# Performance work log

Measured on AMD Instinct MI355X. Metric: run time of the kernel, lower is better.

## Reference

```python
import jax, jax.numpy as jnp
import numpy as np

B, N, C = 2, 2048, 1024
H = 16
D = C // H  # head_dim = 64
SCALE = D ** -0.5


def setup_inputs() -> dict:
    key = jax.random.key(0)
    ks = jax.random.split(key, 9)
    s = C ** -0.5  # ~ torch Linear default init scale
    return {
        "x": jax.random.normal(ks[0], (B, N, C), dtype=jnp.float32),
        "Wq": jax.random.uniform(ks[1], (C, C), jnp.float32, -s, s),
        "bq": jax.random.uniform(ks[2], (C,), jnp.float32, -s, s),
        "Wk": jax.random.uniform(ks[3], (C, C), jnp.float32, -s, s),
        "bk": jax.random.uniform(ks[4], (C,), jnp.float32, -s, s),
        "Wv": jax.random.uniform(ks[5], (C, C), jnp.float32, -s, s),
        "bv": jax.random.uniform(ks[6], (C,), jnp.float32, -s, s),
        "Wo": jax.random.uniform(ks[7], (C, C), jnp.float32, -s, s),
        "bo": jax.random.uniform(ks[8], (C,), jnp.float32, -s, s),
    }


def reference(x, Wq, bq, Wk, bk, Wv, bv, Wo, bo):
    # Projections: [B,N,C] -> [B,H,N,D]
    def split_heads(t):
        return t.reshape(B, N, H, D).transpose(0, 2, 1, 3)

    q = split_heads(x @ Wq.T + bq)
    k = split_heads(x @ Wk.T + bk)
    v = split_heads(x @ Wv.T + bv)

    scores = jnp.einsum("bhnd,bhmd->bhnm", q, k) * SCALE  # [B,H,N,N]
    attn = jax.nn.softmax(scores, axis=-1)
    out = jnp.einsum("bhnm,bhmd->bhnd", attn, v)  # [B,H,N,D]
    out = out.transpose(0, 2, 1, 3).reshape(B, N, C)
    return out @ Wo.T + bo
```

## Files before the change

### kernel.cpp

```cpp
#include <hip/hip_runtime.h>
#include <stdint.h>


typedef _Float16 h8 __attribute__((ext_vector_type(8)));
typedef _Float16 h4 __attribute__((ext_vector_type(4)));
typedef float f4 __attribute__((ext_vector_type(4)));
typedef float f16f __attribute__((ext_vector_type(16)));
typedef uint32_t u32;
typedef u32 u32x4 __attribute__((ext_vector_type(4)));

#define AS1(p) ((const __attribute__((address_space(1))) void*)(p))
#define AS3(p) ((__attribute__((address_space(3))) void*)(p))

template <int ITERS>
__device__ __forceinline__ void stage128B(const _Float16* g, int ldk, _Float16* s, int tid) {
#pragma unroll
  for (int j = 0; j < ITERS; ++j) {
    int off = j * 4096 + tid * 16;
    int row = off >> 7;
    int ch = (off >> 4) & 7;
    int gch = ch ^ (row & 7);
    __builtin_amdgcn_global_load_lds(AS1(g + row * ldk + gch * 8), AS3(s + (off >> 1)), 16, 0, 0);
  }
}

__device__ __forceinline__ void stage_v(const _Float16* g, _Float16* s, int tid) {
#pragma unroll
  for (int j = 0; j < 2; ++j) {
    int off = j * 4096 + tid * 16;
    int row = off >> 7;
    int ch = (off >> 4) & 7;
    int gch = ch ^ (row & 7);
    __builtin_amdgcn_global_load_lds(AS1(g + row * 2048 + gch * 8), AS3(s + (off >> 1)), 16, 0, 0);
  }
}
__device__ __forceinline__ void stage_k(const _Float16* g, _Float16* s, int tid) {
#pragma unroll
  for (int j = 0; j < 2; ++j) {
    int off = j * 4096 + tid * 16;
    int row = off >> 7;
    int ch = (off >> 4) & 7;
    int gch = ch ^ ((row & 3) | ((row >> 1) & 4));
    __builtin_amdgcn_global_load_lds(AS1(g + row * 64 + gch * 8), AS3(s + (off >> 1)), 16, 0, 0);
  }
}

__device__ __forceinline__ h8 frag64(const _Float16* s, int row, int g) {
  return *(const h8*)(s + row * 64 + ((g ^ (row & 7)) << 3));
}

__global__ void cvt_all(const float* __restrict__ x, const float* __restrict__ Wq,
                        const float* __restrict__ Wk, const float* __restrict__ Wv,
                        const float* __restrict__ Wo, _Float16* __restrict__ xh,
                        _Float16* __restrict__ q, _Float16* __restrict__ k,
                        _Float16* __restrict__ v, _Float16* __restrict__ o) {
  int blk = blockIdx.x;
  const float* src; _Float16* dst; int off;
  if (blk < 2048)      { src = x;  dst = xh; off = blk; }
  else if (blk < 2560) { src = Wq; dst = q;  off = blk - 2048; }
  else if (blk < 3072) { src = Wk; dst = k;  off = blk - 2560; }
  else if (blk < 3584) { src = Wv; dst = v;  off = blk - 3072; }
  else                 { src = Wo; dst = o;  off = blk - 3584; }
  int i = off * 2048 + threadIdx.x * 8;
  f4 a = *(const f4*)(src + i);
  f4 b = *(const f4*)(src + i + 4);
  h8 ov;
  ov[0] = (_Float16)a[0]; ov[1] = (_Float16)a[1]; ov[2] = (_Float16)a[2]; ov[3] = (_Float16)a[3];
  ov[4] = (_Float16)b[0]; ov[5] = (_Float16)b[1]; ov[6] = (_Float16)b[2]; ov[7] = (_Float16)b[3];
  *(h8*)(dst + i) = ov;
}

__global__ __launch_bounds__(256, 4) void gemm_qkv(
    const _Float16* __restrict__ X,
    const _Float16* __restrict__ W0, const _Float16* __restrict__ W1, const _Float16* __restrict__ W2,
    const float* __restrict__ b0, const float* __restrict__ b1, const float* __restrict__ b2,
    _Float16* __restrict__ O0, _Float16* __restrict__ O1, _Float16* __restrict__ O2) {
  __shared__ _Float16 As[128 * 64];
  __shared__ _Float16 Bs[64 * 64];

  int flat = blockIdx.x + 16 * (blockIdx.y + 32 * blockIdx.z);
  int nid = (flat & 7) * 192 + (flat >> 3);
  int z = nid >> 9;
  int rem = nid & 511;
  int by = rem >> 4, bx = rem & 15;

  const _Float16* W = (z == 0) ? W0 : (z == 1) ? W1 : W2;
  const float* bias = (z == 0) ? b0 : (z == 1) ? b1 : b2;

  int tid = threadIdx.x;
  int lane = tid & 63, wave = tid >> 6;
  int quad = lane >> 4, l15 = lane & 15;
  int wm = (wave >> 1) << 6, wn = (wave & 1) << 5;
  int m0 = by << 7, n0 = bx << 6;

  f4 acc[4][2] = {};
  for (int k0 = 0; k0 < 1024; k0 += 64) {
    stage128B<4>(X + m0 * 1024 + k0, 1024, As, tid);
    stage128B<2>(W + n0 * 1024 + k0, 1024, Bs, tid);
    __syncthreads();
#pragma unroll
    for (int ks = 0; ks < 2; ++ks) {
      h8 af[4], bf[2];
#pragma unroll
      for (int i = 0; i < 4; ++i) af[i] = frag64(As, wm + i * 16 + l15, ks * 4 + quad);
#pragma unroll
      for (int i = 0; i < 2; ++i) bf[i] = frag64(Bs, wn + i * 16 + l15, ks * 4 + quad);
#pragma unroll
      for (int mi = 0; mi < 4; ++mi)
#pragma unroll
        for (int ni = 0; ni < 2; ++ni)
          acc[mi][ni] = __builtin_amdgcn_mfma_f32_16x16x32_f16(af[mi], bf[ni], acc[mi][ni], 0, 0, 0);
    }
    __syncthreads();
  }

  if (z == 2) {
#pragma unroll
    for (int mi = 0; mi < 4; ++mi) {
#pragma unroll
      for (int ni = 0; ni < 2; ++ni) {
        int o = n0 + wn + ni * 16 + l15;
        float bv = bias[o];
        int h = o >> 6, dd = o & 63;
        int m = m0 + wm + mi * 16 + quad * 4;
        int b = m >> 11, n = m & 2047;
        h4 v;
#pragma unroll
        for (int r = 0; r < 4; ++r) v[r] = (_Float16)(acc[mi][ni][r] + bv);
        *(h4*)(O2 + (((b * 16 + h) * 64 + dd) * 2048 + n)) = v;
      }
    }
  } else {
    float scale = (z == 0) ? 0.125f * 1.44269504089f : 1.0f;
    _Float16* Out = (z == 0) ? O0 : O1;
#pragma unroll
    for (int mi = 0; mi < 4; ++mi) {
#pragma unroll
      for (int ni = 0; ni < 2; ++ni) {
        int o = n0 + wn + ni * 16 + l15;
        float bv = bias[o];
        int h = o >> 6, d = o & 63;
#pragma unroll
        for (int r = 0; r < 4; ++r) {
          int m = m0 + wm + mi * 16 + quad * 4 + r;
          int b = m >> 11, n = m & 2047;
          float v = (acc[mi][ni][r] + bv) * scale;
          Out[(((b * 16 + h) * 2048 + n) << 6) + d] = (_Float16)v;
        }
      }
    }
  }
}

__global__ __launch_bounds__(256, 3) void gemm_out(
    const _Float16* __restrict__ A, const _Float16* __restrict__ W,
    const float* __restrict__ bias, float* __restrict__ Out) {
  __shared__ _Float16 As[128 * 64];
  __shared__ _Float16 Bs[64 * 64];
  int tid = threadIdx.x;
  int lane = tid & 63, wave = tid >> 6;
  int quad = lane >> 4, l15 = lane & 15;
  int wm = (wave >> 1) << 6, wn = (wave & 1) << 5;

  int flat = blockIdx.x + (blockIdx.y << 4);
  int nid = (flat & 7) * 64 + (flat >> 3);
  int n0 = (nid & 15) << 6;
  int m0 = (nid >> 4) << 7;

  f4 acc[4][2] = {};
  for (int k0 = 0; k0 < 1024; k0 += 64) {
    stage128B<4>(A + m0 * 1024 + k0, 1024, As, tid);
    stage128B<2>(W + n0 * 1024 + k0, 1024, Bs, tid);
    __syncthreads();
#pragma unroll
    for (int ks = 0; ks < 2; ++ks) {
      h8 af[4], bf[2];
#pragma unroll
      for (int i = 0; i < 4; ++i) af[i] = frag64(As, wm + i * 16 + l15, ks * 4 + quad);
#pragma unroll
      for (int i = 0; i < 2; ++i) bf[i] = frag64(Bs, wn + i * 16 + l15, ks * 4 + quad);
#pragma unroll
      for (int mi = 0; mi < 4; ++mi)
#pragma unroll
        for (int ni = 0; ni < 2; ++ni)
          acc[mi][ni] = __builtin_amdgcn_mfma_f32_16x16x32_f16(af[mi], bf[ni], acc[mi][ni], 0, 0, 0);
    }
    __syncthreads();
  }
#pragma unroll
  for (int mi = 0; mi < 4; ++mi) {
#pragma unroll
    for (int ni = 0; ni < 2; ++ni) {
      int o = n0 + wn + ni * 16 + l15;
      float bv = bias[o];
#pragma unroll
      for (int r = 0; r < 4; ++r) {
        int m = m0 + wm + mi * 16 + quad * 4 + r;
        Out[m * 1024 + o] = acc[mi][ni][r] + bv;
      }
    }
  }
}

__global__ __launch_bounds__(256, 2) void attn(
    const _Float16* __restrict__ Q, const _Float16* __restrict__ Kv,
    const _Float16* __restrict__ Vt, _Float16* __restrict__ AO) {
  __shared__ _Float16 smem[6 * 4096];
  _Float16* Ksb = smem;
  _Float16* Vsb = smem + 3 * 4096;

  int tid = threadIdx.x, lane = tid & 63, wave = tid >> 6;
  int h = lane >> 5, l31 = lane & 31;
  int p = wave & 1, qg = wave >> 1;

  int flat = blockIdx.y * 16 + blockIdx.x;
  int nid = (flat & 7) * 64 + (flat >> 3);
  int bh = nid >> 4, q0 = (nid & 15) << 7;

  const _Float16* Qb = Q + (bh * 2048 + q0 + qg * 64 + l31) * 64;
  h8 qf[2][4];
#pragma unroll
  for (int qs = 0; qs < 2; ++qs)
#pragma unroll
    for (int ks4 = 0; ks4 < 4; ++ks4)
      qf[qs][ks4] = *(const h8*)(Qb + qs * 32 * 64 + ks4 * 16 + h * 8);

  int krow = (l31 & 19) | ((l31 & 4) << 1) | ((l31 & 8) >> 1);
  int kbase = (p * 32 + krow) * 64;
  int kx = (krow & 3) | ((krow >> 1) & 4);
  int vx = l31 & 7;

  const _Float16* Kb = Kv + bh * 131072;
  const _Float16* Vb = Vt + bh * 131072;
  f16f oacc[2][2] = {};
  float lsum[2] = {0.f, 0.f};

  stage_k(Kb, Ksb, tid);
  stage_v(Vb, Vsb, tid);
  stage_k(Kb + 4096, Ksb + 4096, tid);
  stage_v(Vb + 64, Vsb + 4096, tid);

  int bp = 0;
  for (int ph = 0; ph < 32; ++ph) {
    if (ph < 31) {
      asm volatile("s_waitcnt vmcnt(4)\n\ts_barrier" ::: "memory");
    } else {
      asm volatile("s_waitcnt vmcnt(0)\n\ts_barrier" ::: "memory");
    }
    const _Float16* Kst = Ksb + bp * 4096;
    const _Float16* Vst = Vsb + bp * 4096;

    f16f sacc[2] = {};
#pragma unroll
    for (int ks4 = 0; ks4 < 4; ++ks4) {
      h8 kf = *(const h8*)(Kst + kbase + (((ks4 * 2 + h) ^ kx) << 3));
      sacc[0] = __builtin_amdgcn_mfma_f32_32x32x16_f16(kf, qf[0][ks4], sacc[0], 0, 0, 0);
      sacc[1] = __builtin_amdgcn_mfma_f32_32x32x16_f16(kf, qf[1][ks4], sacc[1], 0, 0, 0);
    }

    u32 pkw[2][8];
#pragma unroll
    for (int qs = 0; qs < 2; ++qs) {
#pragma unroll
      for (int i = 0; i < 8; ++i) {
        float pa = __builtin_amdgcn_exp2f(sacc[qs][2 * i]);
        float pb = __builtin_amdgcn_exp2f(sacc[qs][2 * i + 1]);
        lsum[qs] += pa + pb;
        pkw[qs][i] = __builtin_bit_cast(u32, __builtin_amdgcn_cvt_pkrtz(pa, pb));
      }
    }

#pragma unroll
    for (int s = 0; s < 2; ++s) {
      u32x4 pw0 = {pkw[0][4 * s], pkw[0][4 * s + 1], pkw[0][4 * s + 2], pkw[0][4 * s + 3]};
      u32x4 pw1 = {pkw[1][4 * s], pkw[1][4 * s + 1], pkw[1][4 * s + 2], pkw[1][4 * s + 3]};
      h8 pb0 = __builtin_bit_cast(h8, pw0);
      h8 pb1 = __builtin_bit_cast(h8, pw1);
      int ch = (((p << 2) | (s << 1) | h) ^ vx) << 3;
#pragma unroll
      for (int dt = 0; dt < 2; ++dt) {
        h8 vf = *(const h8*)(Vst + (dt * 32 + l31) * 64 + ch);
        oacc[0][dt] = __builtin_amdgcn_mfma_f32_32x32x16_f16(vf, pb0, oacc[0][dt], 0, 0, 0);
        oacc[1][dt] = __builtin_amdgcn_mfma_f32_32x32x16_f16(vf, pb1, oacc[1][dt], 0, 0, 0);
      }
    }

    if (ph < 30) {
      int sl = bp ? bp - 1 : 2;
      stage_k(Kb + (ph + 2) * 4096, Ksb + sl * 4096, tid);
      stage_v(Vb + (ph + 2) * 64, Vsb + sl * 4096, tid);
    }
    bp = (bp == 2) ? 0 : bp + 1;
  }

  __syncthreads();
  float* cb = (float*)smem;
  if (p) {
    float* w = cb + (qg * 64 + lane) * 66;
#pragma unroll
    for (int qs = 0; qs < 2; ++qs)
#pragma unroll
      for (int dt = 0; dt < 2; ++dt)
#pragma unroll
        for (int i = 0; i < 16; ++i) w[(qs * 2 + dt) * 16 + i] = oacc[qs][dt][i];
    w[64] = lsum[0];
    w[65] = lsum[1];
  }
  __syncthreads();
  if (!p) {
    const float* r = cb + (qg * 64 + lane) * 66;
#pragma unroll
    for (int qs = 0; qs < 2; ++qs)
#pragma unroll
      for (int dt = 0; dt < 2; ++dt)
#pragma unroll
        for (int i = 0; i < 16; ++i) oacc[qs][dt][i] += r[(qs * 2 + dt) * 16 + i];
    lsum[0] += r[64];
    lsum[1] += r[65];

    int b = bh >> 4, hh = bh & 15;
#pragma unroll
    for (int qs = 0; qs < 2; ++qs) {
      float l = lsum[qs] + __shfl_xor(lsum[qs], 32);
      float inv = 1.0f / l;
      int n = q0 + qg * 64 + qs * 32 + l31;
      _Float16* base = AO + (b * 2048 + n) * 1024 + hh * 64;
#pragma unroll
      for (int dt = 0; dt < 2; ++dt) {
#pragma unroll
        for (int b2 = 0; b2 < 4; ++b2) {
          h4 o;
#pragma unroll
          for (int a = 0; a < 4; ++a) o[a] = (_Float16)(oacc[qs][dt][b2 * 4 + a] * inv);
          *(h4*)(base + dt * 32 + b2 * 8 + h * 4) = o;
        }
      }
    }
  }
}

extern "C" void kernel_launch(void* const* d_in, const int* in_sizes, int n_in,
                              void* d_out, int out_size, void* d_ws, size_t ws_size,
                              hipStream_t stream) {
  const float* x = (const float*)d_in[0];
  const float* Wq = (const float*)d_in[1];
  const float* bq = (const float*)d_in[2];
  const float* Wk = (const float*)d_in[3];
  const float* bk = (const float*)d_in[4];
  const float* Wv = (const float*)d_in[5];
  const float* bv = (const float*)d_in[6];
  const float* Wo = (const float*)d_in[7];
  const float* bo = (const float*)d_in[8];
  float* out = (float*)d_out;

  char* w = (char*)d_ws;
  _Float16* xh  = (_Float16*)(w);
  _Float16* Wqh = (_Float16*)(w + (8u << 20));
  _Float16* Wkh = (_Float16*)(w + (10u << 20));
  _Float16* Wvh = (_Float16*)(w + (12u << 20));
  _Float16* Woh = (_Float16*)(w + (14u << 20));
  _Float16* Qh  = (_Float16*)(w + (16u << 20));
  _Float16* Kh  = (_Float16*)(w + (24u << 20));
  _Float16* Vth = (_Float16*)(w + (32u << 20));
  _Float16* AOh = xh;

  cvt_all<<<4096, 256, 0, stream>>>(x, Wq, Wk, Wv, Wo, xh, Wqh, Wkh, Wvh, Woh);
  gemm_qkv<<<dim3(16, 32, 3), 256, 0, stream>>>(xh, Wqh, Wkh, Wvh, bq, bk, bv, Qh, Kh, Vth);
  attn<<<dim3(16, 32), 256, 0, stream>>>(Qh, Kh, Vth, AOh);
  gemm_out<<<dim3(16, 32), 256, 0, stream>>>(AOh, Woh, bo, out);
}
```

Measured before the change: 188.1 us.

## Compute Q, K and V tiles in one block sharing the staged X tile

The QKV projection now has each block load one X tile and three weight tiles, accumulating Q, K and V outputs together instead of launching a separate block per projection. This cuts X tile global loads and LDS staging threefold. In exchange it raises accumulator registers and LDS per block, lowers the occupancy hint from 4 to 2, and shrinks the grid from 1536 to 512 blocks, which may leave fewer waves in flight on a large GPU.

```diff
diff --git a/kernel.cpp b/kernel.cpp
--- a/kernel.cpp
+++ b/kernel.cpp
@@ -70,68 +70,55 @@
   *(h8*)(dst + i) = ov;
 }
 
-__global__ __launch_bounds__(256, 4) void gemm_qkv(
+__global__ __launch_bounds__(256, 2) void gemm_qkv(
     const _Float16* __restrict__ X,
     const _Float16* __restrict__ W0, const _Float16* __restrict__ W1, const _Float16* __restrict__ W2,
     const float* __restrict__ b0, const float* __restrict__ b1, const float* __restrict__ b2,
     _Float16* __restrict__ O0, _Float16* __restrict__ O1, _Float16* __restrict__ O2) {
   __shared__ _Float16 As[128 * 64];
-  __shared__ _Float16 Bs[64 * 64];
-
-  int flat = blockIdx.x + 16 * (blockIdx.y + 32 * blockIdx.z);
-  int nid = (flat & 7) * 192 + (flat >> 3);
-  int z = nid >> 9;
-  int rem = nid & 511;
-  int by = rem >> 4, bx = rem & 15;
-
-  const _Float16* W = (z == 0) ? W0 : (z == 1) ? W1 : W2;
-  const float* bias = (z == 0) ? b0 : (z == 1) ? b1 : b2;
+  __shared__ _Float16 Bs[3][64 * 64];
+
+  int flat = blockIdx.x + (blockIdx.y << 4);
+  int nid = (flat & 7) * 64 + (flat >> 3);
+  int bx = nid & 15, by = nid >> 4;
+  int m0 = by << 7, n0 = bx << 6;
 
   int tid = threadIdx.x;
   int lane = tid & 63, wave = tid >> 6;
   int quad = lane >> 4, l15 = lane & 15;
   int wm = (wave >> 1) << 6, wn = (wave & 1) << 5;
-  int m0 = by << 7, n0 = bx << 6;
-
-  f4 acc[4][2] = {};
+
+  f4 acc[3][4][2] = {};
   for (int k0 = 0; k0 < 1024; k0 += 64) {
     stage128B<4>(X + m0 * 1024 + k0, 1024, As, tid);
-    stage128B<2>(W + n0 * 1024 + k0, 1024, Bs, tid);
+    stage128B<2>(W0 + n0 * 1024 + k0, 1024, Bs[0], tid);
+    stage128B<2>(W1 + n0 * 1024 + k0, 1024, Bs[1], tid);
+    stage128B<2>(W2 + n0 * 1024 + k0, 1024, Bs[2], tid);
     __syncthreads();
 #pragma unroll
     for (int ks = 0; ks < 2; ++ks) {
-      h8 af[4], bf[2];
+      h8 af[4];
 #pragma unroll
       for (int i = 0; i < 4; ++i) af[i] = frag64(As, wm + i * 16 + l15, ks * 4 + quad);
 #pragma unroll
-      for (int i = 0; i < 2; ++i) bf[i] = frag64(Bs, wn + i * 16 + l15, ks * 4 + quad);
-#pragma unroll
-      for (int mi = 0; mi < 4; ++mi)
-#pragma unroll
-        for (int ni = 0; ni < 2; ++ni)
-          acc[mi][ni] = __builtin_amdgcn_mfma_f32_16x16x32_f16(af[mi], bf[ni], acc[mi][ni], 0, 0, 0);
+      for (int z = 0; z < 3; ++z) {
+        h8 bf[2];
+#pragma unroll
+        for (int i = 0; i < 2; ++i) bf[i] = frag64(Bs[z], wn + i * 16 + l15, ks * 4 + quad);
+#pragma unroll
+        for (int mi = 0; mi < 4; ++mi)
+#pragma unroll
+          for (int ni = 0; ni < 2; ++ni)
+            acc[z][mi][ni] = __builtin_amdgcn_mfma_f32_16x16x32_f16(af[mi], bf[ni], acc[z][mi][ni], 0, 0, 0);
+      }
     }
     __syncthreads();
   }
 
-  if (z == 2) {
-#pragma unroll
-    for (int mi = 0; mi < 4; ++mi) {
-#pragma unroll
-      for (int ni = 0; ni < 2; ++ni) {
-        int o = n0 + wn + ni * 16 + l15;
-        float bv = bias[o];
-        int h = o >> 6, dd = o & 63;
-        int m = m0 + wm + mi * 16 + quad * 4;
-        int b = m >> 11, n = m & 2047;
-        h4 v;
-#pragma unroll
-        for (int r = 0; r < 4; ++r) v[r] = (_Float16)(acc[mi][ni][r] + bv);
-        *(h4*)(O2 + (((b * 16 + h) * 64 + dd) * 2048 + n)) = v;
-      }
-    }
-  } else {
+#pragma unroll
+  for (int z = 0; z < 2; ++z) {
     float scale = (z == 0) ? 0.125f * 1.44269504089f : 1.0f;
+    const float* bias = (z == 0) ? b0 : b1;
     _Float16* Out = (z == 0) ? O0 : O1;
 #pragma unroll
     for (int mi = 0; mi < 4; ++mi) {
@@ -144,10 +131,25 @@
         for (int r = 0; r < 4; ++r) {
           int m = m0 + wm + mi * 16 + quad * 4 + r;
           int b = m >> 11, n = m & 2047;
-          float v = (acc[mi][ni][r] + bv) * scale;
+          float v = (acc[z][mi][ni][r] + bv) * scale;
           Out[(((b * 16 + h) * 2048 + n) << 6) + d] = (_Float16)v;
         }
       }
+    }
+  }
+#pragma unroll
+  for (int mi = 0; mi < 4; ++mi) {
+#pragma unroll
+    for (int ni = 0; ni < 2; ++ni) {
+      int o = n0 + wn + ni * 16 + l15;
+      float bv = b2[o];
+      int h = o >> 6, dd = o & 63;
+      int m = m0 + wm + mi * 16 + quad * 4;
+      int b = m >> 11, n = m & 2047;
+      h4 v;
+#pragma unroll
+      for (int r = 0; r < 4; ++r) v[r] = (_Float16)(acc[2][mi][ni][r] + bv);
+      *(h4*)(O2 + (((b * 16 + h) * 64 + dd) * 2048 + n)) = v;
     }
   }
 }
@@ -365,7 +367,7 @@
   _Float16* AOh = xh;
 
   cvt_all<<<4096, 256, 0, stream>>>(x, Wq, Wk, Wv, Wo, xh, Wqh, Wkh, Wvh, Woh);
-  gemm_qkv<<<dim3(16, 32, 3), 256, 0, stream>>>(xh, Wqh, Wkh, Wvh, bq, bk, bv, Qh, Kh, Vth);
+  gemm_qkv<<<dim3(16, 32), 256, 0, stream>>>(xh, Wqh, Wkh, Wvh, bq, bk, bv, Qh, Kh, Vth);
   attn<<<dim3(16, 32), 256, 0, stream>>>(Qh, Kh, Vth, AOh);
   gemm_out<<<dim3(16, 32), 256, 0, stream>>>(AOh, Woh, bo, out);
 }
```

Measured after the change: 178.3 us. 5.2% less time.
